# Kernel optimization log

Measured on AMD Instinct MI355X. Metric: run time of the kernel, lower is better.

The kernel has to match this reference:

```python
import jax, jax.numpy as jnp
import numpy as np

K_GAUSS = 7      # gaussian_kernel_size
K_CONV = 5       # base-kernel conv size
SIGMA_MIN = 0.01
SIGMA_MAX = 1.0


def setup_inputs() -> dict:
    key = jax.random.key(0)
    k1, k2, k3 = jax.random.split(key, 3)
    input_data = jax.random.normal(k1, (8, 3, 224, 224), dtype=jnp.float32)
    foa_xy = jax.random.randint(k2, (8, 2), 0, 224)  # (x=row, y=col) fixation per sample
    weight = jax.random.normal(k3, (64, 3, K_CONV, K_CONV), dtype=jnp.float32) * 0.05
    return {"input_data": input_data, "foa_xy": foa_xy, "weight": weight}


def _extract_patches(x, k):
    # torch.nn.functional.unfold with stride=1, dilation=1, padding=k//2
    # x: (b,c,h,w) -> (b,c,k*k,h*w); patch flat index = ki*k + kj (row-major)
    b, c, h, w = x.shape
    p = k // 2
    xp = jnp.pad(x, ((0, 0), (0, 0), (p, p), (p, p)))
    shifts = [xp[:, :, i:i + h, j:j + w] for i in range(k) for j in range(k)]
    return jnp.stack(shifts, axis=2).reshape(b, c, k * k, h * w)


def _gaussian_modulate(x, foa_xy):
    # GaussianFOAConv2d: per-pixel normalized Gaussian kernel, sigma linear in distance from FOA
    b, c, h, w = x.shape
    hw = h * w
    ii, jj = jnp.meshgrid(jnp.arange(h, dtype=jnp.float32),
                          jnp.arange(w, dtype=jnp.float32), indexing='ij')
    xy = jnp.stack([ii, jj], axis=-1).reshape(hw, 2)           # (hw,2): (row, col)
    foa = foa_xy.astype(jnp.float32)                            # (b,2)
    dists = jnp.linalg.norm(xy[None, :, :] - foa[:, None, :], axis=-1)
    dists = dists / np.float32(np.sqrt(h ** 2 + w ** 2))        # (b,hw) in [0,1]
    sigmas = (1.0 - dists) * SIGMA_MIN + dists * SIGMA_MAX      # (b,hw)
    r = jnp.arange(-(K_GAUSS // 2), K_GAUSS // 2 + 1, dtype=jnp.float32)
    d2 = (r[:, None] ** 2 + r[None, :] ** 2).reshape(-1)        # (kk,) row-major, matches patch order
    kern = jnp.exp(-d2[None, :, None] / (2.0 * sigmas[:, None, :] ** 2))  # (b,kk,hw)
    kern = kern / jnp.sum(kern, axis=1, keepdims=True)
    patches = _extract_patches(x, K_GAUSS)                      # (b,c,kk,hw)
    out = jnp.einsum('bckp,bkp->bcp', patches, kern)            # spatial-only kernel -> sum over kk
    return out.reshape(b, c, h, w)


def reference(input_data, foa_xy, weight):
    # 1) Gaussian input modulation driven by FOA distance
    modulated = _gaussian_modulate(input_data, foa_xy)
    # 2) classic convolution with the learnable base kernel (stride 1, 'same' padding, no bias)
    p = K_CONV // 2
    return jax.lax.conv_general_dilated(
        modulated, weight, window_strides=(1, 1), padding=((p, p), (p, p)),
        dimension_numbers=('NCHW', 'OIHW', 'NCHW'))
```

## Files before the change

kernel.cpp:

```cpp
#include <hip/hip_runtime.h>

#define H 224
#define W 224
#define HW (224 * 224)
#define CIN 3
#define OCH 64
#define TLW 32
#define TLH 4
#define MODW 40
#define RAWW 44
#define STGW 136

typedef __attribute__((ext_vector_type(8))) short short8;
typedef __attribute__((ext_vector_type(4))) float f32x4;

__device__ __forceinline__ unsigned f2bf_pk(float lo, float hi) {
    unsigned a = __float_as_uint(lo), b = __float_as_uint(hi);
    a = (a + 0x7FFFu + ((a >> 16) & 1u)) >> 16;
    b = (b + 0x7FFFu + ((b >> 16) & 1u)) & 0xFFFF0000u;
    return a | b;
}

__global__ void make_wfrag(const float* __restrict__ w, uint4* __restrict__ wB) {
    int t = threadIdx.x;
    if (t >= 768) return;
    int lane = t & 63;
    int nt = (t >> 6) & 3;
    int ks = t >> 8;
    int q = lane >> 4;
    int n = nt * 16 + (lane & 15);
    float v[8];
#pragma unroll
    for (int j = 0; j < 8; ++j) {
        int kk = q * 8 + j;
        v[j] = (kk < 25) ? w[n * 75 + ks * 25 + kk] : 0.f;
    }
    uint4 r;
    r.x = f2bf_pk(v[0], v[1]);
    r.y = f2bf_pk(v[2], v[3]);
    r.z = f2bf_pk(v[4], v[5]);
    r.w = f2bf_pk(v[6], v[7]);
    wB[(ks * 4 + nt) * 64 + lane] = r;
}

__global__ __launch_bounds__(256, 4) void fused_mfma(
    const float* __restrict__ in, const int* __restrict__ foa,
    const uint4* __restrict__ wB, float* __restrict__ out)
{
    __shared__ float s_mod[CIN][TLH + 4][MODW];
    __shared__ __align__(16) char s_un[16 * STGW * 4];

    const int tid = threadIdx.x;
    const int tx0 = blockIdx.x * TLW;
    const int ty0 = blockIdx.y * TLH;
    const int b = blockIdx.z;

    {
        float (*s_raw)[TLH + 10][RAWW] = (float (*)[TLH + 10][RAWW])s_un;
        const float* src = in + (size_t)b * CIN * HW;
        for (int i = tid; i < CIN * (TLH + 10) * 42; i += 256) {
            int ch = i / ((TLH + 10) * 42);
            int rem = i - ch * ((TLH + 10) * 42);
            int rr = rem / 42;
            int cc = rem - rr * 42;
            int gr = ty0 - 5 + rr, gc = tx0 - 5 + cc;
            float v = 0.f;
            if ((unsigned)gr < H && (unsigned)gc < W) v = src[ch * HW + gr * W + gc];
            s_raw[ch][rr][cc] = v;
        }
    }
    __syncthreads();

    {
        float (*s_raw)[TLH + 10][RAWW] = (float (*)[TLH + 10][RAWW])s_un;
        float fr = (float)foa[2 * b + 0], fc = (float)foa[2 * b + 1];
        for (int p = tid; p < (TLH + 4) * 36; p += 256) {
            int mr = p / 36, mc = p - mr * 36;
            int gr = ty0 - 2 + mr, gc = tx0 - 2 + mc;
            bool inimg = ((unsigned)gr < H) && ((unsigned)gc < W);
            float dr = (float)gr - fr, dc = (float)gc - fc;
            float dist = sqrtf(dr * dr + dc * dc) * 3.1567268e-3f;
            float sigma = 0.01f + 0.99f * dist;
            float ae = -0.5f / (sigma * sigma);
            float e1 = __expf(ae);
            float e2 = e1 * e1, e4 = e2 * e2, e9 = e4 * e4 * e1;
            float pw[7] = {e9, e4, e1, 1.f, e1, e4, e9};
            float S = 1.f + 2.f * (e1 + e4 + e9);
            float inv = 1.f / (S * S);
#pragma unroll
            for (int ch = 0; ch < CIN; ++ch) {
                float a = 0.f;
#pragma unroll
                for (int ki = 0; ki < 7; ++ki) {
                    const float* rp = &s_raw[ch][mr + ki][mc];
                    float rs = 0.f;
#pragma unroll
                    for (int kj = 0; kj < 7; ++kj) rs += pw[kj] * rp[kj];
                    a += pw[ki] * rs;
                }
                s_mod[ch][mr][mc] = inimg ? a * inv : 0.f;
            }
        }
    }
    __syncthreads();

    const int lane = tid & 63;
    const int wv = tid >> 6;
    const int q = lane >> 4;
    const int li = lane & 15;

    int aoff[8];
#pragma unroll
    for (int j = 0; j < 8; ++j) {
        int kk = q * 8 + j;
        int kkc = kk > 24 ? 24 : kk;
        int ky = (kkc * 13) >> 6;
        int kx = kkc - ky * 5;
        aoff[j] = ky * (MODW * 4) + kx * 4;
    }
    int abase[2];
#pragma unroll
    for (int mt = 0; mt < 2; ++mt) {
        int mti = wv * 2 + mt;
        int py = mti >> 1;
        int x = (mti & 1) * 16 + li;
        abase[mt] = py * (MODW * 4) + x * 4;
    }
    const char* modb = (const char*)&s_mod[0][0][0];
    const bool qv = (q < 3);

    f32x4 acc[2][4];
#pragma unroll
    for (int mt = 0; mt < 2; ++mt)
#pragma unroll
        for (int nt = 0; nt < 4; ++nt) acc[mt][nt] = (f32x4){0.f, 0.f, 0.f, 0.f};

#pragma unroll
    for (int ks = 0; ks < 3; ++ks) {
        short8 bf[4];
#pragma unroll
        for (int nt = 0; nt < 4; ++nt) {
            union { uint4 u4; short8 s8; } cv;
            cv.u4 = wB[(ks * 4 + nt) * 64 + lane];
            bf[nt] = cv.s8;
        }
#pragma unroll
        for (int mt = 0; mt < 2; ++mt) {
            float v[8];
#pragma unroll
            for (int j = 0; j < 8; ++j) {
                float x = *(const float*)(modb + (abase[mt] + aoff[j] + ks * (8 * MODW * 4)));
                v[j] = (j == 0 || qv) ? x : 0.f;
            }
            union { unsigned u[4]; short8 s8; } af;
            af.u[0] = f2bf_pk(v[0], v[1]);
            af.u[1] = f2bf_pk(v[2], v[3]);
            af.u[2] = f2bf_pk(v[4], v[5]);
            af.u[3] = f2bf_pk(v[6], v[7]);
#pragma unroll
            for (int nt = 0; nt < 4; ++nt)
                acc[mt][nt] = __builtin_amdgcn_mfma_f32_16x16x32_bf16(
                    af.s8, bf[nt], acc[mt][nt], 0, 0, 0);
        }
    }

    float (*stg)[STGW] = (float (*)[STGW])s_un;
#pragma unroll 1
    for (int nt = 0; nt < 4; ++nt) {
        __syncthreads();
#pragma unroll
        for (int mt = 0; mt < 2; ++mt) {
            int mti = wv * 2 + mt;
            int m0 = (mti >> 1) * 32 + (mti & 1) * 16 + q * 4;
            *(f32x4*)&stg[li][m0] = acc[mt][nt];
        }
        __syncthreads();
#pragma unroll
        for (int i = 0; i < 2; ++i) {
            int ocl = (tid >> 5) + 8 * i;
            int m4 = (tid & 31);
            f32x4 val = *(const f32x4*)&stg[ocl][m4 * 4];
            int py = (m4 * 4) >> 5;
            int x = (m4 * 4) & 31;
            float* op = out + (((size_t)b * OCH + nt * 16 + ocl) * H + (ty0 + py)) * W
                      + tx0 + x;
            *(f32x4*)op = val;
        }
    }
}

extern "C" void kernel_launch(void* const* d_in, const int* in_sizes, int n_in,
                              void* d_out, int out_size, void* d_ws, size_t ws_size,
                              hipStream_t stream) {
    const float* input  = (const float*)d_in[0];
    const int*   foa    = (const int*)d_in[1];
    const float* weight = (const float*)d_in[2];
    float* outp = (float*)d_out;
    uint4* wB   = (uint4*)d_ws;

    make_wfrag<<<1, 768, 0, stream>>>(weight, wB);

    dim3 grid(W / TLW, H / TLH, 8);
    fused_mfma<<<grid, 256, 0, stream>>>(input, foa, wB, outp);
}
```

Before: 142.9 us.

## Split fused kernel into modulate pass and padded-buffer MFMA conv pass

Replaces the single fused kernel, which recomputed the Gaussian modulation over a halo for each small tile, with a separate modulate kernel that writes a zero-padded modulated image to workspace. A new gemm kernel then reads that buffer straight from global memory with weights as the MFMA A operand held in registers, so no shared-memory staging or extra syncs are needed. This removes the halo recompute and the LDS transpose. In exchange it adds a memset, an extra launch, a global round trip of the intermediate, and uncoalesced 16-wide scalar output stores.

```diff
diff --git a/kernel.cpp b/kernel.cpp
--- a/kernel.cpp
+++ b/kernel.cpp
@@ -5,11 +5,10 @@
 #define HW (224 * 224)
 #define CIN 3
 #define OCH 64
-#define TLW 32
-#define TLH 4
-#define MODW 40
-#define RAWW 44
-#define STGW 136
+#define PW 228
+#define PHW (PW * PW)
+#define MTW 32
+#define MTH 16
 
 typedef __attribute__((ext_vector_type(8))) short short8;
 typedef __attribute__((ext_vector_type(4))) float f32x4;
@@ -21,170 +20,145 @@
     return a | b;
 }
 
-__global__ void make_wfrag(const float* __restrict__ w, uint4* __restrict__ wB) {
+__global__ void make_wA(const float* __restrict__ w, uint4* __restrict__ wA) {
     int t = threadIdx.x;
     if (t >= 768) return;
     int lane = t & 63;
-    int nt = (t >> 6) & 3;
-    int ks = t >> 8;
+    int fi = t >> 6;
+    int mt = fi / 3, ks = fi - mt * 3;
     int q = lane >> 4;
-    int n = nt * 16 + (lane & 15);
+    int oc = mt * 16 + (lane & 15);
     float v[8];
 #pragma unroll
     for (int j = 0; j < 8; ++j) {
         int kk = q * 8 + j;
-        v[j] = (kk < 25) ? w[n * 75 + ks * 25 + kk] : 0.f;
+        v[j] = (kk < 25) ? w[oc * 75 + ks * 25 + kk] : 0.f;
     }
     uint4 r;
     r.x = f2bf_pk(v[0], v[1]);
     r.y = f2bf_pk(v[2], v[3]);
     r.z = f2bf_pk(v[4], v[5]);
     r.w = f2bf_pk(v[6], v[7]);
-    wB[(ks * 4 + nt) * 64 + lane] = r;
+    wA[fi * 64 + lane] = r;
 }
 
-__global__ __launch_bounds__(256, 4) void fused_mfma(
+__global__ __launch_bounds__(256) void modulate(
     const float* __restrict__ in, const int* __restrict__ foa,
-    const uint4* __restrict__ wB, float* __restrict__ out)
+    float* __restrict__ Pm)
 {
-    __shared__ float s_mod[CIN][TLH + 4][MODW];
-    __shared__ __align__(16) char s_un[16 * STGW * 4];
+    __shared__ float s_raw[CIN][MTH + 6][40];
 
-    const int tid = threadIdx.x;
-    const int tx0 = blockIdx.x * TLW;
-    const int ty0 = blockIdx.y * TLH;
-    const int b = blockIdx.z;
+    int tx0 = blockIdx.x * MTW;
+    int ty0 = blockIdx.y * MTH;
+    int b = blockIdx.z;
+    int tid = threadIdx.x;
 
-    {
-        float (*s_raw)[TLH + 10][RAWW] = (float (*)[TLH + 10][RAWW])s_un;
-        const float* src = in + (size_t)b * CIN * HW;
-        for (int i = tid; i < CIN * (TLH + 10) * 42; i += 256) {
-            int ch = i / ((TLH + 10) * 42);
-            int rem = i - ch * ((TLH + 10) * 42);
-            int rr = rem / 42;
-            int cc = rem - rr * 42;
-            int gr = ty0 - 5 + rr, gc = tx0 - 5 + cc;
-            float v = 0.f;
-            if ((unsigned)gr < H && (unsigned)gc < W) v = src[ch * HW + gr * W + gc];
-            s_raw[ch][rr][cc] = v;
-        }
+    const float* src = in + (size_t)b * CIN * HW;
+    for (int i = tid; i < CIN * 22 * 38; i += 256) {
+        int ch = i / (22 * 38);
+        int rem = i - ch * (22 * 38);
+        int rr = rem / 38;
+        int cc = rem - rr * 38;
+        int gr = ty0 - 3 + rr, gc = tx0 - 3 + cc;
+        float v = 0.f;
+        if ((unsigned)gr < H && (unsigned)gc < W) v = src[ch * HW + gr * W + gc];
+        s_raw[ch][rr][cc] = v;
     }
     __syncthreads();
 
-    {
-        float (*s_raw)[TLH + 10][RAWW] = (float (*)[TLH + 10][RAWW])s_un;
-        float fr = (float)foa[2 * b + 0], fc = (float)foa[2 * b + 1];
-        for (int p = tid; p < (TLH + 4) * 36; p += 256) {
-            int mr = p / 36, mc = p - mr * 36;
-            int gr = ty0 - 2 + mr, gc = tx0 - 2 + mc;
-            bool inimg = ((unsigned)gr < H) && ((unsigned)gc < W);
-            float dr = (float)gr - fr, dc = (float)gc - fc;
-            float dist = sqrtf(dr * dr + dc * dc) * 3.1567268e-3f;
-            float sigma = 0.01f + 0.99f * dist;
-            float ae = -0.5f / (sigma * sigma);
-            float e1 = __expf(ae);
-            float e2 = e1 * e1, e4 = e2 * e2, e9 = e4 * e4 * e1;
-            float pw[7] = {e9, e4, e1, 1.f, e1, e4, e9};
-            float S = 1.f + 2.f * (e1 + e4 + e9);
-            float inv = 1.f / (S * S);
+    float fr = (float)foa[2 * b + 0], fc = (float)foa[2 * b + 1];
+    for (int p = tid; p < MTH * MTW; p += 256) {
+        int r = p >> 5, c = p & 31;
+        int gr = ty0 + r, gc = tx0 + c;
+        float dr = (float)gr - fr, dc = (float)gc - fc;
+        float dist = sqrtf(dr * dr + dc * dc) * 3.1567268e-3f;
+        float sigma = 0.01f + 0.99f * dist;
+        float ae = -0.5f / (sigma * sigma);
+        float e1 = __expf(ae);
+        float e2 = e1 * e1, e4 = e2 * e2, e9 = e4 * e4 * e1;
+        float pw[7] = {e9, e4, e1, 1.f, e1, e4, e9};
+        float S = 1.f + 2.f * (e1 + e4 + e9);
+        float inv = 1.f / (S * S);
 #pragma unroll
-            for (int ch = 0; ch < CIN; ++ch) {
-                float a = 0.f;
+        for (int ch = 0; ch < CIN; ++ch) {
+            float a = 0.f;
 #pragma unroll
-                for (int ki = 0; ki < 7; ++ki) {
-                    const float* rp = &s_raw[ch][mr + ki][mc];
-                    float rs = 0.f;
+            for (int ki = 0; ki < 7; ++ki) {
+                const float* rp = &s_raw[ch][r + ki][c];
+                float rs = 0.f;
 #pragma unroll
-                    for (int kj = 0; kj < 7; ++kj) rs += pw[kj] * rp[kj];
-                    a += pw[ki] * rs;
-                }
-                s_mod[ch][mr][mc] = inimg ? a * inv : 0.f;
+                for (int kj = 0; kj < 7; ++kj) rs += pw[kj] * rp[kj];
+                a += pw[ki] * rs;
             }
+            Pm[(size_t)(b * CIN + ch) * PHW + (size_t)(gr + 2) * PW + (gc + 2)] = a * inv;
         }
     }
-    __syncthreads();
+}
 
-    const int lane = tid & 63;
-    const int wv = tid >> 6;
-    const int q = lane >> 4;
-    const int li = lane & 15;
+__global__ __launch_bounds__(256, 4) void gemm(
+    const uint4* __restrict__ wA, const float* __restrict__ Pm,
+    float* __restrict__ out)
+{
+    int tid = threadIdx.x;
+    int lane = tid & 63;
+    int wv = tid >> 6;
+    int q = lane >> 4, li = lane & 15;
 
-    int aoff[8];
+    int px0 = blockIdx.x * 16;
+    int py = blockIdx.y * 4 + wv;
+    int b = blockIdx.z;
+
+    short8 aw[4][3];
+#pragma unroll
+    for (int mt = 0; mt < 4; ++mt)
+#pragma unroll
+        for (int ks = 0; ks < 3; ++ks) {
+            union { uint4 u4; short8 s8; } cv;
+            cv.u4 = wA[(mt * 3 + ks) * 64 + lane];
+            aw[mt][ks] = cv.s8;
+        }
+
+    int ofs[8];
 #pragma unroll
     for (int j = 0; j < 8; ++j) {
         int kk = q * 8 + j;
         int kkc = kk > 24 ? 24 : kk;
         int ky = (kkc * 13) >> 6;
         int kx = kkc - ky * 5;
-        aoff[j] = ky * (MODW * 4) + kx * 4;
+        ofs[j] = ky * PW + kx;
     }
-    int abase[2];
+
+    short8 bf[3];
 #pragma unroll
-    for (int mt = 0; mt < 2; ++mt) {
-        int mti = wv * 2 + mt;
-        int py = mti >> 1;
-        int x = (mti & 1) * 16 + li;
-        abase[mt] = py * (MODW * 4) + x * 4;
+    for (int ks = 0; ks < 3; ++ks) {
+        const float* p = Pm + (size_t)(b * CIN + ks) * PHW + (size_t)py * PW + px0 + li;
+        float v[8];
+#pragma unroll
+        for (int j = 0; j < 8; ++j) v[j] = p[ofs[j]];
+        union { unsigned u[4]; short8 s8; } cv;
+        cv.u[0] = f2bf_pk(v[0], v[1]);
+        cv.u[1] = f2bf_pk(v[2], v[3]);
+        cv.u[2] = f2bf_pk(v[4], v[5]);
+        cv.u[3] = f2bf_pk(v[6], v[7]);
+        bf[ks] = cv.s8;
     }
-    const char* modb = (const char*)&s_mod[0][0][0];
-    const bool qv = (q < 3);
 
-    f32x4 acc[2][4];
+    f32x4 acc[4];
 #pragma unroll
-    for (int mt = 0; mt < 2; ++mt)
+    for (int mt = 0; mt < 4; ++mt) acc[mt] = (f32x4){0.f, 0.f, 0.f, 0.f};
 #pragma unroll
-        for (int nt = 0; nt < 4; ++nt) acc[mt][nt] = (f32x4){0.f, 0.f, 0.f, 0.f};
+    for (int ks = 0; ks < 3; ++ks)
+#pragma unroll
+        for (int mt = 0; mt < 4; ++mt)
+            acc[mt] = __builtin_amdgcn_mfma_f32_16x16x32_bf16(
+                aw[mt][ks], bf[ks], acc[mt], 0, 0, 0);
 
 #pragma unroll
-    for (int ks = 0; ks < 3; ++ks) {
-        short8 bf[4];
+    for (int mt = 0; mt < 4; ++mt) {
 #pragma unroll
-        for (int nt = 0; nt < 4; ++nt) {
-            union { uint4 u4; short8 s8; } cv;
-            cv.u4 = wB[(ks * 4 + nt) * 64 + lane];
-            bf[nt] = cv.s8;
-        }
-#pragma unroll
-        for (int mt = 0; mt < 2; ++mt) {
-            float v[8];
-#pragma unroll
-            for (int j = 0; j < 8; ++j) {
-                float x = *(const float*)(modb + (abase[mt] + aoff[j] + ks * (8 * MODW * 4)));
-                v[j] = (j == 0 || qv) ? x : 0.f;
-            }
-            union { unsigned u[4]; short8 s8; } af;
-            af.u[0] = f2bf_pk(v[0], v[1]);
-            af.u[1] = f2bf_pk(v[2], v[3]);
-            af.u[2] = f2bf_pk(v[4], v[5]);
-            af.u[3] = f2bf_pk(v[6], v[7]);
-#pragma unroll
-            for (int nt = 0; nt < 4; ++nt)
-                acc[mt][nt] = __builtin_amdgcn_mfma_f32_16x16x32_bf16(
-                    af.s8, bf[nt], acc[mt][nt], 0, 0, 0);
-        }
-    }
-
-    float (*stg)[STGW] = (float (*)[STGW])s_un;
-#pragma unroll 1
-    for (int nt = 0; nt < 4; ++nt) {
-        __syncthreads();
-#pragma unroll
-        for (int mt = 0; mt < 2; ++mt) {
-            int mti = wv * 2 + mt;
-            int m0 = (mti >> 1) * 32 + (mti & 1) * 16 + q * 4;
-            *(f32x4*)&stg[li][m0] = acc[mt][nt];
-        }
-        __syncthreads();
-#pragma unroll
-        for (int i = 0; i < 2; ++i) {
-            int ocl = (tid >> 5) + 8 * i;
-            int m4 = (tid & 31);
-            f32x4 val = *(const f32x4*)&stg[ocl][m4 * 4];
-            int py = (m4 * 4) >> 5;
-            int x = (m4 * 4) & 31;
-            float* op = out + (((size_t)b * OCH + nt * 16 + ocl) * H + (ty0 + py)) * W
-                      + tx0 + x;
-            *(f32x4*)op = val;
+        for (int r = 0; r < 4; ++r) {
+            int oc = mt * 16 + q * 4 + r;
+            out[(size_t)(b * OCH + oc) * HW + (size_t)py * W + px0 + li] = acc[mt][r];
         }
     }
 }
@@ -196,10 +170,17 @@
     const int*   foa    = (const int*)d_in[1];
     const float* weight = (const float*)d_in[2];
     float* outp = (float*)d_out;
-    uint4* wB   = (uint4*)d_ws;
 
-    make_wfrag<<<1, 768, 0, stream>>>(weight, wB);
+    uint4* wA = (uint4*)d_ws;
+    float* Pm = (float*)((char*)d_ws + 16384);
 
-    dim3 grid(W / TLW, H / TLH, 8);
-    fused_mfma<<<grid, 256, 0, stream>>>(input, foa, wB, outp);
+    hipMemsetAsync(Pm, 0, (size_t)8 * CIN * PHW * sizeof(float), stream);
+
+    make_wA<<<1, 768, 0, stream>>>(weight, wA);
+
+    dim3 gridM(W / MTW, H / MTH, 8);
+    modulate<<<gridM, 256, 0, stream>>>(input, foa, Pm);
+
+    dim3 gridG(14, 56, 8);
+    gemm<<<gridG, 256, 0, stream>>>(wA, Pm, outp);
 }
```

After: 137.3 us. 3.9% less time.
